# Optimization experiments

Measured on AMD Instinct MI355X. Metric: run time of the kernel, lower is better.

The kernel has to match this reference:

```python
import jax, jax.numpy as jnp
import numpy as np

ACT_BW = 8
PAR_BW = 4
EPS = 1e-8

def fake_quant(t, bw):
    # symmetric per-tensor fake quantization with dynamic absmax observer
    qmax = float(2 ** (bw - 1) - 1)
    scale = jnp.maximum(jnp.max(jnp.abs(t)) / qmax, EPS)
    q = jnp.clip(jnp.round(t / scale), -qmax, qmax) * scale
    # straight-through estimator (matches torch fake-quant backward)
    return t + jax.lax.stop_gradient(q - t)

def setup_inputs() -> dict:
    key = jax.random.key(0)
    k1, k2, k3 = jax.random.split(key, 3)
    tokens, d_in, d_out = 4096, 4096, 4096
    x = jax.random.normal(k1, (tokens, d_in), dtype=jnp.float32)
    # kaiming-uniform-ish init scale
    bound_w = 1.0 / np.sqrt(d_in)
    weight = jax.random.uniform(k2, (d_out, d_in), dtype=jnp.float32, minval=-bound_w, maxval=bound_w)
    b = jax.random.uniform(k3, (d_out,), dtype=jnp.float32, minval=-bound_w, maxval=bound_w)
    return {"x": x, "weight": weight, "b": b}

def reference(x, weight, b):
    # 1) requantize input activations (act_bitwidth)
    xq = fake_quant(x, ACT_BW)
    # 2) quantize weight (par_bitwidth), transpose [out,in] -> [in,out]
    wq = fake_quant(weight, PAR_BW).T
    # 3) quantize bias (act_bitwidth)
    bq = fake_quant(b, ACT_BW)
    # 4) AddMM: bias + x @ w^T, then requantize the output (multiplier's quantizer)
    out = bq + jnp.matmul(xq, wq)  # [tokens, out_features]
    return fake_quant(out, ACT_BW)
```

## Files before the change

### kernel.cpp

```cpp
#include <hip/hip_runtime.h>

#define NELEM (4096 * 4096)
#define KDIM 4096
#define NDIM 4096
#define DOUT 4096
#define EPSQ 1e-8f
#define STRIDE_MEM (2048 * 256)

typedef __attribute__((ext_vector_type(4))) int i32x4;

typedef __attribute__((address_space(3))) void lds_void;
typedef const __attribute__((address_space(1))) void gbl_void;

__device__ __forceinline__ void load_lds16(const void* g, void* l) {
    __builtin_amdgcn_global_load_lds((gbl_void*)g, (lds_void*)l, 16, 0, 0);
}

__device__ __forceinline__ float wave_max64(float v) {
#pragma unroll
    for (int off = 32; off > 0; off >>= 1)
        v = fmaxf(v, __shfl_down(v, off));
    return v;
}

__global__ __launch_bounds__(256) void absmax_xwb(
    const float4* __restrict__ x, const float4* __restrict__ w,
    const float* __restrict__ b, unsigned* __restrict__ amax)
{
    float mx = 0.f, mw = 0.f;
    int i = blockIdx.x * 256 + threadIdx.x;
#pragma unroll
    for (int it = 0; it < 8; ++it, i += STRIDE_MEM) {
        float4 a = x[i];
        float4 c = w[i];
        mx = fmaxf(mx, fmaxf(fmaxf(fabsf(a.x), fabsf(a.y)), fmaxf(fabsf(a.z), fabsf(a.w))));
        mw = fmaxf(mw, fmaxf(fmaxf(fabsf(c.x), fabsf(c.y)), fmaxf(fabsf(c.z), fabsf(c.w))));
    }
    float mb = 0.f;
    if (blockIdx.x == 0) {
#pragma unroll
        for (int t = 0; t < DOUT / 256; ++t)
            mb = fmaxf(mb, fabsf(b[t * 256 + threadIdx.x]));
    }

    mx = wave_max64(mx); mw = wave_max64(mw); mb = wave_max64(mb);
    __shared__ float red[3][4];
    const int wave = threadIdx.x >> 6, lane = threadIdx.x & 63;
    if (lane == 0) { red[0][wave] = mx; red[1][wave] = mw; red[2][wave] = mb; }
    __syncthreads();
    if (threadIdx.x == 0) {
        float r0 = fmaxf(fmaxf(red[0][0], red[0][1]), fmaxf(red[0][2], red[0][3]));
        float r1 = fmaxf(fmaxf(red[1][0], red[1][1]), fmaxf(red[1][2], red[1][3]));
        atomicMax(&amax[0], __float_as_uint(r0));
        atomicMax(&amax[1], __float_as_uint(r1));
        if (blockIdx.x == 0) {
            float r2 = fmaxf(fmaxf(red[2][0], red[2][1]), fmaxf(red[2][2], red[2][3]));
            atomicMax(&amax[2], __float_as_uint(r2));
        }
    }
}

__device__ __forceinline__ int pack4(float4 a, float s, float qmax) {
    int b0 = (int)fminf(fmaxf(rintf(a.x / s), -qmax), qmax);
    int b1 = (int)fminf(fmaxf(rintf(a.y / s), -qmax), qmax);
    int b2 = (int)fminf(fmaxf(rintf(a.z / s), -qmax), qmax);
    int b3 = (int)fminf(fmaxf(rintf(a.w / s), -qmax), qmax);
    return (b0 & 0xff) | ((b1 & 0xff) << 8) | ((b2 & 0xff) << 16) | (b3 << 24);
}

__global__ __launch_bounds__(256) void quant_xwb(
    const float4* __restrict__ x, const float4* __restrict__ w,
    const float* __restrict__ b, const unsigned* __restrict__ amax,
    int4* __restrict__ qx, int4* __restrict__ qw, float* __restrict__ bq)
{
    const float sx = fmaxf(__uint_as_float(amax[0]) / 127.0f, EPSQ);
    const float sw = fmaxf(__uint_as_float(amax[1]) / 7.0f, EPSQ);
    int i = blockIdx.x * 256 + threadIdx.x;
#pragma unroll
    for (int it = 0; it < 2; ++it, i += STRIDE_MEM) {
        int4 r;
        r.x = pack4(x[i * 4 + 0], sx, 127.f);
        r.y = pack4(x[i * 4 + 1], sx, 127.f);
        r.z = pack4(x[i * 4 + 2], sx, 127.f);
        r.w = pack4(x[i * 4 + 3], sx, 127.f);
        qx[i] = r;
        int4 p;
        p.x = pack4(w[i * 4 + 0], sw, 7.f);
        p.y = pack4(w[i * 4 + 1], sw, 7.f);
        p.z = pack4(w[i * 4 + 2], sw, 7.f);
        p.w = pack4(w[i * 4 + 3], sw, 7.f);
        qw[i] = p;
    }
    if (blockIdx.x == 0) {
        const float sb = fmaxf(__uint_as_float(amax[2]) / 127.0f, EPSQ);
#pragma unroll
        for (int t = 0; t < DOUT / 256; ++t) {
            int j = t * 256 + threadIdx.x;
            float q = fminf(fmaxf(rintf(b[j] / sb), -127.f), 127.f);
            bq[j] = q * sb;
        }
    }
}

__global__ __launch_bounds__(256, 2) void gemm_i8(
    const char* __restrict__ qx,
    const char* __restrict__ qw,
    const float* __restrict__ bq,
    const unsigned* __restrict__ amax,
    float* __restrict__ out,
    unsigned* __restrict__ amax_out)
{
    constexpr int K = KDIM, N = NDIM, BK = 64;
    __shared__ char smemA[128 * BK];
    __shared__ char smemB[128 * BK];
    __shared__ float red[4];

    const int tid = threadIdx.x;
    const int wave = tid >> 6;
    const int lane = tid & 63;
    const int bm = blockIdx.y, bn = blockIdx.x;

    const int wm = (wave & 1) * 64;
    const int wn = (wave >> 1) * 64;

    i32x4 acc[4][4] = {};

    const int srow = wave * 16 + (lane >> 2);
    const int scol = (((lane & 3) ^ ((lane >> 3) & 3)) << 4);
    const char* aP0 = qx + (long)(bm * 128 + srow) * K + scol;
    const char* aP1 = aP0 + 64 * K;
    const char* bP0 = qw + (long)(bn * 128 + srow) * K + scol;
    const char* bP1 = bP0 + 64 * K;
    char* aL0 = smemA + wave * 1024;
    char* aL1 = aL0 + 4096;
    char* bL0 = smemB + wave * 1024;
    char* bL1 = bL0 + 4096;

    const int frow = lane & 15;
    const int fks = (((lane >> 4) ^ ((frow >> 1) & 3)) << 4);

    for (int k0 = 0; k0 < K; k0 += BK) {
        __syncthreads();
        load_lds16(aP0 + k0, aL0);
        load_lds16(aP1 + k0, aL1);
        load_lds16(bP0 + k0, bL0);
        load_lds16(bP1 + k0, bL1);
        __syncthreads();

        i32x4 af[4], bf[4];
#pragma unroll
        for (int i = 0; i < 4; ++i)
            af[i] = *(const i32x4*)(smemA + (wm + i * 16 + frow) * BK + fks);
#pragma unroll
        for (int j = 0; j < 4; ++j)
            bf[j] = *(const i32x4*)(smemB + (wn + j * 16 + frow) * BK + fks);
#pragma unroll
        for (int i = 0; i < 4; ++i)
#pragma unroll
            for (int j = 0; j < 4; ++j)
                acc[i][j] = __builtin_amdgcn_mfma_i32_16x16x64_i8(af[i], bf[j], acc[i][j], 0, 0, 0);
    }

    const float sx = fmaxf(__uint_as_float(amax[0]) / 127.0f, EPSQ);
    const float sw = fmaxf(__uint_as_float(amax[1]) / 7.0f, EPSQ);
    const float s = sx * sw;
    const int col = lane & 15;
    const int rbase = (lane >> 4) * 4;
    float am = 0.f;
    float bqv[4];
#pragma unroll
    for (int j = 0; j < 4; ++j) bqv[j] = bq[bn * 128 + wn + j * 16 + col];

#pragma unroll
    for (int i = 0; i < 4; ++i) {
#pragma unroll
        for (int r = 0; r < 4; ++r) {
            const int m = bm * 128 + wm + i * 16 + rbase + r;
            float* orow = out + (long)m * N + bn * 128 + wn + col;
#pragma unroll
            for (int j = 0; j < 4; ++j) {
                float o = fmaf(s, (float)acc[i][j][r], bqv[j]);
                am = fmaxf(am, fabsf(o));
                orow[j * 16] = o;
            }
        }
    }
    am = wave_max64(am);
    if (lane == 0) red[wave] = am;
    __syncthreads();
    if (tid == 0)
        atomicMax(amax_out, __float_as_uint(fmaxf(fmaxf(red[0], red[1]), fmaxf(red[2], red[3]))));
}

__global__ __launch_bounds__(256) void final_quant(
    float4* __restrict__ out, const unsigned* __restrict__ amax)
{
    const float so = fmaxf(__uint_as_float(amax[3]) / 127.0f, EPSQ);
    int i = blockIdx.x * 256 + threadIdx.x;
#pragma unroll
    for (int it = 0; it < 8; ++it, i += STRIDE_MEM) {
        float4 v = out[i];
        v.x = fminf(fmaxf(rintf(v.x / so), -127.f), 127.f) * so;
        v.y = fminf(fmaxf(rintf(v.y / so), -127.f), 127.f) * so;
        v.z = fminf(fmaxf(rintf(v.z / so), -127.f), 127.f) * so;
        v.w = fminf(fmaxf(rintf(v.w / so), -127.f), 127.f) * so;
        out[i] = v;
    }
}

extern "C" void kernel_launch(void* const* d_in, const int* in_sizes, int n_in,
                              void* d_out, int out_size, void* d_ws, size_t ws_size,
                              hipStream_t stream) {
    const float* x = (const float*)d_in[0];
    const float* w = (const float*)d_in[1];
    const float* b = (const float*)d_in[2];
    float* out = (float*)d_out;

    char* ws = (char*)d_ws;
    unsigned* amax = (unsigned*)ws;
    float* bq = (float*)(ws + 256);
    char* qx = (char*)(ws + 32768);
    char* qw = (char*)(ws + 32768 + (size_t)NELEM);

    hipMemsetAsync(amax, 0, 16, stream);
    hipLaunchKernelGGL(absmax_xwb, dim3(2048), dim3(256), 0, stream,
                       (const float4*)x, (const float4*)w, b, amax);
    hipLaunchKernelGGL(quant_xwb, dim3(2048), dim3(256), 0, stream,
                       (const float4*)x, (const float4*)w, b, amax,
                       (int4*)qx, (int4*)qw, bq);
    hipLaunchKernelGGL(gemm_i8, dim3(32, 32), dim3(256), 0, stream,
                       qx, qw, bq, amax, out, amax + 3);
    hipLaunchKernelGGL(final_quant, dim3(2048), dim3(256), 0, stream,
                       (float4*)out, amax);
}
```

Measured before the change: 300.4 us.

## Fuse output requantization into GEMM via cooperative grid sync

Replaces the separate GEMM and final requantization passes with a cooperative-launch GEMM. Each block reduces its output absmax, syncs across the grid, then quantizes its accumulators in registers and writes the output only once. This removes the full read-modify-write pass over the 64MB fp32 output. The quant kernel is also rewritten to pack one float4 per thread per iteration instead of four. The cooperative launch needs all 1024 blocks resident at once, with up to 4 per CU, and falls back to the old path if the launch fails.

```diff
diff --git a/kernel.cpp b/kernel.cpp
--- a/kernel.cpp
+++ b/kernel.cpp
@@ -1,4 +1,5 @@
 #include <hip/hip_runtime.h>
+#include <hip/hip_cooperative_groups.h>
 
 #define NELEM (4096 * 4096)
 #define KDIM 4096
@@ -71,25 +72,15 @@
 __global__ __launch_bounds__(256) void quant_xwb(
     const float4* __restrict__ x, const float4* __restrict__ w,
     const float* __restrict__ b, const unsigned* __restrict__ amax,
-    int4* __restrict__ qx, int4* __restrict__ qw, float* __restrict__ bq)
+    int* __restrict__ qx, int* __restrict__ qw, float* __restrict__ bq)
 {
     const float sx = fmaxf(__uint_as_float(amax[0]) / 127.0f, EPSQ);
     const float sw = fmaxf(__uint_as_float(amax[1]) / 7.0f, EPSQ);
     int i = blockIdx.x * 256 + threadIdx.x;
 #pragma unroll
-    for (int it = 0; it < 2; ++it, i += STRIDE_MEM) {
-        int4 r;
-        r.x = pack4(x[i * 4 + 0], sx, 127.f);
-        r.y = pack4(x[i * 4 + 1], sx, 127.f);
-        r.z = pack4(x[i * 4 + 2], sx, 127.f);
-        r.w = pack4(x[i * 4 + 3], sx, 127.f);
-        qx[i] = r;
-        int4 p;
-        p.x = pack4(w[i * 4 + 0], sw, 7.f);
-        p.y = pack4(w[i * 4 + 1], sw, 7.f);
-        p.z = pack4(w[i * 4 + 2], sw, 7.f);
-        p.w = pack4(w[i * 4 + 3], sw, 7.f);
-        qw[i] = p;
+    for (int it = 0; it < 8; ++it, i += STRIDE_MEM) {
+        qx[i] = pack4(x[i], sx, 127.f);
+        qw[i] = pack4(w[i], sw, 7.f);
     }
     if (blockIdx.x == 0) {
         const float sb = fmaxf(__uint_as_float(amax[2]) / 127.0f, EPSQ);
@@ -102,23 +93,20 @@
     }
 }
 
-__global__ __launch_bounds__(256, 2) void gemm_i8(
-    const char* __restrict__ qx,
-    const char* __restrict__ qw,
-    const float* __restrict__ bq,
-    const unsigned* __restrict__ amax,
-    float* __restrict__ out,
-    unsigned* __restrict__ amax_out)
+__global__ __launch_bounds__(256, 4) void gemm_i8_coop(
+    const char* __restrict__ qx, const char* __restrict__ qw,
+    const float* __restrict__ bq, const unsigned* __restrict__ amax,
+    float* __restrict__ out, unsigned* __restrict__ amax_out)
 {
     constexpr int K = KDIM, N = NDIM, BK = 64;
     __shared__ char smemA[128 * BK];
     __shared__ char smemB[128 * BK];
-    __shared__ float red[4];
 
     const int tid = threadIdx.x;
     const int wave = tid >> 6;
     const int lane = tid & 63;
-    const int bm = blockIdx.y, bn = blockIdx.x;
+    const int bid = blockIdx.x;
+    const int bm = bid >> 5, bn = bid & 31;
 
     const int wm = (wave & 1) * 64;
     const int wn = (wave >> 1) * 64;
@@ -172,6 +160,112 @@
     for (int j = 0; j < 4; ++j) bqv[j] = bq[bn * 128 + wn + j * 16 + col];
 
 #pragma unroll
+    for (int i = 0; i < 4; ++i)
+#pragma unroll
+        for (int r = 0; r < 4; ++r)
+#pragma unroll
+            for (int j = 0; j < 4; ++j) {
+                float o = fmaf(s, (float)acc[i][j][r], bqv[j]);
+                am = fmaxf(am, fabsf(o));
+            }
+    am = wave_max64(am);
+
+    __syncthreads();
+    float* red = (float*)smemA;
+    if (lane == 0) red[wave] = am;
+    __syncthreads();
+    if (tid == 0)
+        atomicMax(amax_out, __float_as_uint(fmaxf(fmaxf(red[0], red[1]), fmaxf(red[2], red[3]))));
+
+    cooperative_groups::this_grid().sync();
+
+    if (tid == 0)
+        red[4] = fmaxf(__uint_as_float(atomicMax(amax_out, 0u)) / 127.0f, EPSQ);
+    __syncthreads();
+    const float so = red[4];
+
+#pragma unroll
+    for (int i = 0; i < 4; ++i)
+#pragma unroll
+        for (int r = 0; r < 4; ++r) {
+            const int m = bm * 128 + wm + i * 16 + rbase + r;
+            float* orow = out + (long)m * N + bn * 128 + wn + col;
+#pragma unroll
+            for (int j = 0; j < 4; ++j) {
+                float o = fmaf(s, (float)acc[i][j][r], bqv[j]);
+                float q = fminf(fmaxf(rintf(o / so), -127.f), 127.f);
+                orow[j * 16] = q * so;
+            }
+        }
+}
+
+__global__ __launch_bounds__(256, 2) void gemm_i8(
+    const char* __restrict__ qx, const char* __restrict__ qw,
+    const float* __restrict__ bq, const unsigned* __restrict__ amax,
+    float* __restrict__ out, unsigned* __restrict__ amax_out)
+{
+    constexpr int K = KDIM, N = NDIM, BK = 64;
+    __shared__ char smemA[128 * BK];
+    __shared__ char smemB[128 * BK];
+    __shared__ float red[4];
+
+    const int tid = threadIdx.x;
+    const int wave = tid >> 6;
+    const int lane = tid & 63;
+    const int bm = blockIdx.y, bn = blockIdx.x;
+
+    const int wm = (wave & 1) * 64;
+    const int wn = (wave >> 1) * 64;
+
+    i32x4 acc[4][4] = {};
+
+    const int srow = wave * 16 + (lane >> 2);
+    const int scol = (((lane & 3) ^ ((lane >> 3) & 3)) << 4);
+    const char* aP0 = qx + (long)(bm * 128 + srow) * K + scol;
+    const char* aP1 = aP0 + 64 * K;
+    const char* bP0 = qw + (long)(bn * 128 + srow) * K + scol;
+    const char* bP1 = bP0 + 64 * K;
+    char* aL0 = smemA + wave * 1024;
+    char* aL1 = aL0 + 4096;
+    char* bL0 = smemB + wave * 1024;
+    char* bL1 = bL0 + 4096;
+
+    const int frow = lane & 15;
+    const int fks = (((lane >> 4) ^ ((frow >> 1) & 3)) << 4);
+
+    for (int k0 = 0; k0 < K; k0 += BK) {
+        __syncthreads();
+        load_lds16(aP0 + k0, aL0);
+        load_lds16(aP1 + k0, aL1);
+        load_lds16(bP0 + k0, bL0);
+        load_lds16(bP1 + k0, bL1);
+        __syncthreads();
+
+        i32x4 af[4], bf[4];
+#pragma unroll
+        for (int i = 0; i < 4; ++i)
+            af[i] = *(const i32x4*)(smemA + (wm + i * 16 + frow) * BK + fks);
+#pragma unroll
+        for (int j = 0; j < 4; ++j)
+            bf[j] = *(const i32x4*)(smemB + (wn + j * 16 + frow) * BK + fks);
+#pragma unroll
+        for (int i = 0; i < 4; ++i)
+#pragma unroll
+            for (int j = 0; j < 4; ++j)
+                acc[i][j] = __builtin_amdgcn_mfma_i32_16x16x64_i8(af[i], bf[j], acc[i][j], 0, 0, 0);
+    }
+
+    const float sx = fmaxf(__uint_as_float(amax[0]) / 127.0f, EPSQ);
+    const float sw = fmaxf(__uint_as_float(amax[1]) / 7.0f, EPSQ);
+    const float s = sx * sw;
+    const int col = lane & 15;
+    const int rbase = (lane >> 4) * 4;
+    float am = 0.f;
+    float bqv[4];
+#pragma unroll
+    for (int j = 0; j < 4; ++j) bqv[j] = bq[bn * 128 + wn + j * 16 + col];
+
+#pragma unroll
     for (int i = 0; i < 4; ++i) {
 #pragma unroll
         for (int r = 0; r < 4; ++r) {
@@ -227,9 +321,24 @@
                        (const float4*)x, (const float4*)w, b, amax);
     hipLaunchKernelGGL(quant_xwb, dim3(2048), dim3(256), 0, stream,
                        (const float4*)x, (const float4*)w, b, amax,
-                       (int4*)qx, (int4*)qw, bq);
-    hipLaunchKernelGGL(gemm_i8, dim3(32, 32), dim3(256), 0, stream,
-                       qx, qw, bq, amax, out, amax + 3);
-    hipLaunchKernelGGL(final_quant, dim3(2048), dim3(256), 0, stream,
-                       (float4*)out, amax);
-}
+                       (int*)qx, (int*)qw, bq);
+
+    const char* qxp = (const char*)qx;
+    const char* qwp = (const char*)qw;
+    const float* bqp = bq;
+    const unsigned* amaxp = amax;
+    float* outp = out;
+    unsigned* amax3 = amax + 3;
+    void* kargs[] = {(void*)&qxp, (void*)&qwp, (void*)&bqp, (void*)&amaxp,
+                     (void*)&outp, (void*)&amax3};
+    hipError_t cerr = hipLaunchCooperativeKernel(
+        reinterpret_cast<const void*>(gemm_i8_coop),
+        dim3(1024), dim3(256), kargs, 0, stream);
+    if (cerr != hipSuccess) {
+        (void)hipGetLastError();
+        hipLaunchKernelGGL(gemm_i8, dim3(32, 32), dim3(256), 0, stream,
+                           (const char*)qx, (const char*)qw, bq, amax, out, amax + 3);
+        hipLaunchKernelGGL(final_quant, dim3(2048), dim3(256), 0, stream,
+                           (float4*)out, amax);
+    }
+}
```

Measured after the change: 445.5 us. 1.48x slower.

## Rewrite int8 GEMM as 256x256-tile, 8-wave, 4-stage pipelined kernel

Applied to the files above, without the earlier changes.

Replaces the 128x128 single-buffered int8 MFMA GEMM with a 256x256 tile per 512-thread block. It uses a 4-deep LDS ring fed by direct global-to-LDS loads, explicit vmcnt waits with a single barrier per K step, s_setprio around the MFMA cluster, and an XCD-aware block swizzle. This is meant to hide global load latency and raise data reuse per byte loaded. The quant kernel is also changed so each thread packs one float4 into one int per iteration. The 128 KB LDS footprint and larger accumulator set limit occupancy to one block per CU.

```diff
diff --git a/kernel.cpp b/kernel.cpp
--- a/kernel.cpp
+++ b/kernel.cpp
@@ -71,25 +71,15 @@
 __global__ __launch_bounds__(256) void quant_xwb(
     const float4* __restrict__ x, const float4* __restrict__ w,
     const float* __restrict__ b, const unsigned* __restrict__ amax,
-    int4* __restrict__ qx, int4* __restrict__ qw, float* __restrict__ bq)
+    int* __restrict__ qx, int* __restrict__ qw, float* __restrict__ bq)
 {
     const float sx = fmaxf(__uint_as_float(amax[0]) / 127.0f, EPSQ);
     const float sw = fmaxf(__uint_as_float(amax[1]) / 7.0f, EPSQ);
     int i = blockIdx.x * 256 + threadIdx.x;
 #pragma unroll
-    for (int it = 0; it < 2; ++it, i += STRIDE_MEM) {
-        int4 r;
-        r.x = pack4(x[i * 4 + 0], sx, 127.f);
-        r.y = pack4(x[i * 4 + 1], sx, 127.f);
-        r.z = pack4(x[i * 4 + 2], sx, 127.f);
-        r.w = pack4(x[i * 4 + 3], sx, 127.f);
-        qx[i] = r;
-        int4 p;
-        p.x = pack4(w[i * 4 + 0], sw, 7.f);
-        p.y = pack4(w[i * 4 + 1], sw, 7.f);
-        p.z = pack4(w[i * 4 + 2], sw, 7.f);
-        p.w = pack4(w[i * 4 + 3], sw, 7.f);
-        qw[i] = p;
+    for (int it = 0; it < 8; ++it, i += STRIDE_MEM) {
+        qx[i] = pack4(x[i], sx, 127.f);
+        qw[i] = pack4(w[i], sw, 7.f);
     }
     if (blockIdx.x == 0) {
         const float sb = fmaxf(__uint_as_float(amax[2]) / 127.0f, EPSQ);
@@ -102,7 +92,7 @@
     }
 }
 
-__global__ __launch_bounds__(256, 2) void gemm_i8(
+__global__ __launch_bounds__(512, 2) void gemm_i8_8p(
     const char* __restrict__ qx,
     const char* __restrict__ qw,
     const float* __restrict__ bq,
@@ -110,56 +100,62 @@
     float* __restrict__ out,
     unsigned* __restrict__ amax_out)
 {
-    constexpr int K = KDIM, N = NDIM, BK = 64;
-    __shared__ char smemA[128 * BK];
-    __shared__ char smemB[128 * BK];
-    __shared__ float red[4];
+    constexpr int K = KDIM, N = NDIM;
+    __shared__ char lds[131072];
+    char* ldsA = lds;
+    char* ldsB = lds + 65536;
 
     const int tid = threadIdx.x;
-    const int wave = tid >> 6;
-    const int lane = tid & 63;
-    const int bm = blockIdx.y, bn = blockIdx.x;
-
-    const int wm = (wave & 1) * 64;
-    const int wn = (wave >> 1) * 64;
-
-    i32x4 acc[4][4] = {};
-
-    const int srow = wave * 16 + (lane >> 2);
-    const int scol = (((lane & 3) ^ ((lane >> 3) & 3)) << 4);
-    const char* aP0 = qx + (long)(bm * 128 + srow) * K + scol;
-    const char* aP1 = aP0 + 64 * K;
-    const char* bP0 = qw + (long)(bn * 128 + srow) * K + scol;
-    const char* bP1 = bP0 + 64 * K;
-    char* aL0 = smemA + wave * 1024;
-    char* aL1 = aL0 + 4096;
-    char* bL0 = smemB + wave * 1024;
-    char* bL1 = bL0 + 4096;
+    const int wave = tid >> 6, lane = tid & 63;
+    const int swz = (blockIdx.x & 7) * 32 + (blockIdx.x >> 3);
+    const int bm = swz >> 4, bn = swz & 15;
+    const int wm2 = wave >> 2;
+    const int wn4 = wave & 3;
+
+    const int sg16 = (((lane & 3) ^ ((lane >> 3) & 3)) << 4);
+    const char* aG = qx + (size_t)(bm * 256 + wave * 16 + (lane >> 2)) * K + sg16;
+    const char* bG = qw + (size_t)(bn * 256 + wave * 16 + (lane >> 2)) * K + sg16;
 
     const int frow = lane & 15;
     const int fks = (((lane >> 4) ^ ((frow >> 1) & 3)) << 4);
-
-    for (int k0 = 0; k0 < K; k0 += BK) {
-        __syncthreads();
-        load_lds16(aP0 + k0, aL0);
-        load_lds16(aP1 + k0, aL1);
-        load_lds16(bP0 + k0, bL0);
-        load_lds16(bP1 + k0, bL1);
-        __syncthreads();
-
-        i32x4 af[4], bf[4];
-#pragma unroll
-        for (int i = 0; i < 4; ++i)
-            af[i] = *(const i32x4*)(smemA + (wm + i * 16 + frow) * BK + fks);
-#pragma unroll
-        for (int j = 0; j < 4; ++j)
-            bf[j] = *(const i32x4*)(smemB + (wn + j * 16 + frow) * BK + fks);
-#pragma unroll
-        for (int i = 0; i < 4; ++i)
-#pragma unroll
-            for (int j = 0; j < 4; ++j)
-                acc[i][j] = __builtin_amdgcn_mfma_i32_16x16x64_i8(af[i], bf[j], acc[i][j], 0, 0, 0);
-    }
+    const int aoff = (wm2 * 128 + frow) * 64 + fks;
+    const int boff = (wn4 * 64 + frow) * 64 + fks;
+
+    i32x4 acc[8][4] = {};
+
+#define STAGE8(s) { const int p_ = (s) & 3;                                                  \
+    load_lds16(aG + (size_t)(s) * 64,                  ldsA + p_ * 16384 + wave * 1024);     \
+    load_lds16(aG + (size_t)128 * K + (size_t)(s) * 64, ldsA + p_ * 16384 + 8192 + wave * 1024); \
+    load_lds16(bG + (size_t)(s) * 64,                  ldsB + p_ * 16384 + wave * 1024);     \
+    load_lds16(bG + (size_t)128 * K + (size_t)(s) * 64, ldsB + p_ * 16384 + 8192 + wave * 1024); }
+
+#define PHASE8(s, VMN, DO_ST) {                                                              \
+    asm volatile("s_waitcnt vmcnt(%0)" :: "n"(VMN) : "memory");                              \
+    __builtin_amdgcn_s_barrier();                                                            \
+    __builtin_amdgcn_sched_barrier(0);                                                       \
+    if (DO_ST) STAGE8((s) + 3);                                                              \
+    const char* Ab = ldsA + ((s) & 3) * 16384 + aoff;                                        \
+    const char* Bb = ldsB + ((s) & 3) * 16384 + boff;                                        \
+    i32x4 af[8], bf[4];                                                                      \
+    _Pragma("unroll") for (int mi = 0; mi < 8; ++mi)                                         \
+        af[mi] = *(const i32x4*)(Ab + mi * 1024);                                            \
+    _Pragma("unroll") for (int ni = 0; ni < 4; ++ni)                                         \
+        bf[ni] = *(const i32x4*)(Bb + ni * 1024);                                            \
+    __builtin_amdgcn_s_setprio(1);                                                           \
+    _Pragma("unroll") for (int mi = 0; mi < 8; ++mi)                                         \
+    _Pragma("unroll") for (int ni = 0; ni < 4; ++ni)                                         \
+        acc[mi][ni] = __builtin_amdgcn_mfma_i32_16x16x64_i8(af[mi], bf[ni], acc[mi][ni], 0, 0, 0); \
+    __builtin_amdgcn_s_setprio(0); }
+
+    STAGE8(0); STAGE8(1); STAGE8(2);
+
+    for (int s = 0; s < 61; ++s) PHASE8(s, 8, true);
+    PHASE8(61, 8, false);
+    PHASE8(62, 4, false);
+    PHASE8(63, 0, false);
+
+#undef PHASE8
+#undef STAGE8
 
     const float sx = fmaxf(__uint_as_float(amax[0]) / 127.0f, EPSQ);
     const float sw = fmaxf(__uint_as_float(amax[1]) / 7.0f, EPSQ);
@@ -169,27 +165,31 @@
     float am = 0.f;
     float bqv[4];
 #pragma unroll
-    for (int j = 0; j < 4; ++j) bqv[j] = bq[bn * 128 + wn + j * 16 + col];
-
-#pragma unroll
-    for (int i = 0; i < 4; ++i) {
-#pragma unroll
-        for (int r = 0; r < 4; ++r) {
-            const int m = bm * 128 + wm + i * 16 + rbase + r;
-            float* orow = out + (long)m * N + bn * 128 + wn + col;
-#pragma unroll
-            for (int j = 0; j < 4; ++j) {
-                float o = fmaf(s, (float)acc[i][j][r], bqv[j]);
+    for (int ni = 0; ni < 4; ++ni) bqv[ni] = bq[bn * 256 + wn4 * 64 + ni * 16 + col];
+
+#pragma unroll
+    for (int mi = 0; mi < 8; ++mi) {
+#pragma unroll
+        for (int rr = 0; rr < 4; ++rr) {
+            const int m = bm * 256 + wm2 * 128 + mi * 16 + rbase + rr;
+            float* orow = out + (size_t)m * N + bn * 256 + wn4 * 64 + col;
+#pragma unroll
+            for (int ni = 0; ni < 4; ++ni) {
+                float o = fmaf(s, (float)acc[mi][ni][rr], bqv[ni]);
                 am = fmaxf(am, fabsf(o));
-                orow[j * 16] = o;
+                orow[ni * 16] = o;
             }
         }
     }
     am = wave_max64(am);
+    float* red = (float*)lds;
     if (lane == 0) red[wave] = am;
     __syncthreads();
-    if (tid == 0)
-        atomicMax(amax_out, __float_as_uint(fmaxf(fmaxf(red[0], red[1]), fmaxf(red[2], red[3]))));
+    if (tid == 0) {
+        float r = fmaxf(fmaxf(fmaxf(red[0], red[1]), fmaxf(red[2], red[3])),
+                        fmaxf(fmaxf(red[4], red[5]), fmaxf(red[6], red[7])));
+        atomicMax(amax_out, __float_as_uint(r));
+    }
 }
 
 __global__ __launch_bounds__(256) void final_quant(
@@ -227,9 +227,9 @@
                        (const float4*)x, (const float4*)w, b, amax);
     hipLaunchKernelGGL(quant_xwb, dim3(2048), dim3(256), 0, stream,
                        (const float4*)x, (const float4*)w, b, amax,
-                       (int4*)qx, (int4*)qw, bq);
-    hipLaunchKernelGGL(gemm_i8, dim3(32, 32), dim3(256), 0, stream,
-                       qx, qw, bq, amax, out, amax + 3);
+                       (int*)qx, (int*)qw, bq);
+    hipLaunchKernelGGL(gemm_i8_8p, dim3(256), dim3(512), 0, stream,
+                       (const char*)qx, (const char*)qw, bq, amax, out, amax + 3);
     hipLaunchKernelGGL(final_quant, dim3(2048), dim3(256), 0, stream,
                        (float4*)out, amax);
 }
```

Result: faster. 280.4 us (-6.6%).
